# Optimization experiments

Hardware: AMD Instinct MI355X
Metric: run time of the kernel (lower is better)

Reference implementation:

```python
import jax, jax.numpy as jnp
import numpy as np

VOCAB = 50000
B, T, D_OUT = 32, 512, 256
E_DIMS = (300, 300, 200)


def setup_inputs() -> dict:
    key = jax.random.key(0)
    ks = jax.random.split(key, 8)
    ids = jax.random.randint(ks[0], (B, T), 0, VOCAB)
    E0 = jax.random.normal(ks[1], (VOCAB, E_DIMS[0]), dtype=jnp.float32)
    E1 = jax.random.normal(ks[2], (VOCAB, E_DIMS[1]), dtype=jnp.float32)
    E2 = jax.random.normal(ks[3], (VOCAB, E_DIMS[2]), dtype=jnp.float32)
    # Glorot-ish scaled projection weights
    W0 = jax.random.normal(ks[4], (E_DIMS[0], D_OUT), dtype=jnp.float32) / np.sqrt(E_DIMS[0])
    W1 = jax.random.normal(ks[5], (E_DIMS[1], D_OUT), dtype=jnp.float32) / np.sqrt(E_DIMS[1])
    W2 = jax.random.normal(ks[6], (E_DIMS[2], D_OUT), dtype=jnp.float32) / np.sqrt(E_DIMS[2])
    Wa = jax.random.normal(ks[7], (D_OUT, 1), dtype=jnp.float32) / np.sqrt(D_OUT)
    return {
        "ids": ids,
        "E0": E0, "E1": E1, "E2": E2,
        "W0": W0, "b0": jnp.zeros((D_OUT,), jnp.float32),
        "W1": W1, "b1": jnp.zeros((D_OUT,), jnp.float32),
        "W2": W2, "b2": jnp.zeros((D_OUT,), jnp.float32),
        "Wa": Wa, "ba": jnp.zeros((1,), jnp.float32),
    }


def reference(ids, E0, E1, E2, W0, b0, W1, b1, W2, b2, Wa, ba):
    # Per-source embedding gather + Dense projection -> [B, T, D_OUT]
    p0 = E0[ids] @ W0 + b0
    p1 = E1[ids] @ W1 + b1
    p2 = E2[ids] @ W2 + b2
    projected = jnp.stack([p0, p1, p2], axis=2)  # [B, T, n_emb, D]
    # Attention Dense(1) over D, softmax over the n_emb axis
    logits = jnp.einsum('btnd,do->btno', projected, Wa) + ba  # [B, T, n, 1]
    alphas = jax.nn.softmax(logits, axis=2)
    # Weighted combine: matmul(projected^T, alphas) then squeeze -> [B, T, D]
    out = jnp.einsum('btnd,btn->btd', projected, alphas[..., 0])
    return out
```

## Files before the change

### kernel.cpp

```cpp
#include <hip/hip_runtime.h>
#include <hip/hip_bf16.h>

typedef __attribute__((ext_vector_type(8))) short short8;
typedef __attribute__((ext_vector_type(4))) float floatx4;
typedef unsigned short ushort_t;
typedef unsigned int uint_t;

#define DOUT   256
#define KPAD   864
#define XPITCH 872
#define TB     32
#define NTOK   16384

static __device__ inline ushort_t f2bf(float f) {
    union { float f; uint_t u; } a; a.f = f;
    uint_t u = a.u;
    return (ushort_t)((u + 0x7FFFu + ((u >> 16) & 1u)) >> 16);
}
static __device__ inline uint_t pack2bf(float x, float y) {
    return (uint_t)f2bf(x) | ((uint_t)f2bf(y) << 16);
}

__global__ __launch_bounds__(64) void k_prep_u(
    const float* __restrict__ W0, const float* __restrict__ W1,
    const float* __restrict__ W2,
    const float* __restrict__ b0, const float* __restrict__ b1,
    const float* __restrict__ b2,
    const float* __restrict__ Wa, const float* __restrict__ ba,
    float* __restrict__ u, float* __restrict__ lb)
{
    int kp = blockIdx.x;
    int lane = threadIdx.x;
    const float* row = nullptr;
    if (kp < 320)       { if (kp < 300) row = W0 + kp * DOUT; }
    else if (kp < 640)  { int o = kp - 320; if (o < 300) row = W1 + o * DOUT; }
    else if (kp < 864)  { int o = kp - 640; if (o < 200) row = W2 + o * DOUT; }
    else                { int n = kp - 864; row = (n == 0) ? b0 : ((n == 1) ? b1 : b2); }
    float acc = 0.f;
    if (row) {
        for (int j = lane; j < DOUT; j += 64)
            acc += row[j] * Wa[j];
    }
    for (int off = 32; off > 0; off >>= 1) acc += __shfl_down(acc, off);
    if (lane == 0) {
        if (kp < 864) u[kp] = acc;
        else          lb[kp - 864] = acc + ba[0];
    }
}

__global__ __launch_bounds__(256) void k_prep_t(
    const float* __restrict__ W0, const float* __restrict__ W1,
    const float* __restrict__ W2, ushort_t* __restrict__ Wt)
{
    __shared__ ushort_t tile[32][256];
    int tid = threadIdx.x;
    int k0 = blockIdx.x * 32;
    for (int idx = tid; idx < 32 * 256; idx += 256) {
        int kk = idx >> 8, d = idx & 255;
        int kp = k0 + kk;
        float v = 0.f;
        const float* src = nullptr;
        if (kp < 320)      { if (kp < 300) src = W0 + kp * DOUT; }
        else if (kp < 640) { int o = kp - 320; if (o < 300) src = W1 + o * DOUT; }
        else               { int o = kp - 640; if (o < 200) src = W2 + o * DOUT; }
        if (src) v = src[d];
        tile[kk][d] = f2bf(v);
    }
    __syncthreads();
    int d = tid;
    #pragma unroll
    for (int g = 0; g < 4; ++g) {
        union { uint4 v; ushort_t s[8]; } p;
        #pragma unroll
        for (int j = 0; j < 8; ++j) p.s[j] = tile[g * 8 + j][d];
        *(uint4*)(Wt + (size_t)d * KPAD + k0 + g * 8) = p.v;
    }
}

#define MFMA_STEP(ACC, KC) {                                                   \
    short8 a0 = *(const short8*)&Xs[mrow][(KC) + kg8];                         \
    short8 a1 = *(const short8*)&Xs[16 + mrow][(KC) + kg8];                    \
    short8 bv0 = *(const short8*)(bp0 + (KC));                                 \
    short8 bv1 = *(const short8*)(bp1 + (KC));                                 \
    short8 bv2 = *(const short8*)(bp2 + (KC));                                 \
    short8 bv3 = *(const short8*)(bp3 + (KC));                                 \
    ACC[0][0] = __builtin_amdgcn_mfma_f32_16x16x32_bf16(a0, bv0, ACC[0][0], 0, 0, 0); \
    ACC[1][0] = __builtin_amdgcn_mfma_f32_16x16x32_bf16(a1, bv0, ACC[1][0], 0, 0, 0); \
    ACC[0][1] = __builtin_amdgcn_mfma_f32_16x16x32_bf16(a0, bv1, ACC[0][1], 0, 0, 0); \
    ACC[1][1] = __builtin_amdgcn_mfma_f32_16x16x32_bf16(a1, bv1, ACC[1][1], 0, 0, 0); \
    ACC[0][2] = __builtin_amdgcn_mfma_f32_16x16x32_bf16(a0, bv2, ACC[0][2], 0, 0, 0); \
    ACC[1][2] = __builtin_amdgcn_mfma_f32_16x16x32_bf16(a1, bv2, ACC[1][2], 0, 0, 0); \
    ACC[0][3] = __builtin_amdgcn_mfma_f32_16x16x32_bf16(a0, bv3, ACC[0][3], 0, 0, 0); \
    ACC[1][3] = __builtin_amdgcn_mfma_f32_16x16x32_bf16(a1, bv3, ACC[1][3], 0, 0, 0); \
}

__global__ __launch_bounds__(256, 2) void k_main(
    const int* __restrict__ ids,
    const float* __restrict__ E0, const float* __restrict__ E1,
    const float* __restrict__ E2,
    const float* __restrict__ b0, const float* __restrict__ b1,
    const float* __restrict__ b2,
    const float* __restrict__ u, const float* __restrict__ lb,
    const ushort_t* __restrict__ Wt,
    float* __restrict__ out)
{
    __shared__ __align__(16) ushort_t Xs[TB][XPITCH];
    __shared__ float uS[KPAD];
    __shared__ float alphaS[TB][4];

    int tid = threadIdx.x;
    int tok0 = blockIdx.x * TB;

    for (int i = tid; i < KPAD; i += 256) uS[i] = u[i];

    int trow = tid >> 3, sub = tid & 7;
    int id = ids[tok0 + trow];
    uint_t* Xd = (uint_t*)&Xs[trow][0];
    const float2* E0v = (const float2*)E0;
    const float2* E1v = (const float2*)E1;
    const float2* E2v = (const float2*)E2;
    for (int i = sub; i < 150; i += 8) { float2 t = E0v[(size_t)id * 150 + i]; Xd[i]       = pack2bf(t.x, t.y); }
    for (int i = sub; i < 150; i += 8) { float2 t = E1v[(size_t)id * 150 + i]; Xd[160 + i] = pack2bf(t.x, t.y); }
    for (int i = sub; i < 100; i += 8) { float2 t = E2v[(size_t)id * 100 + i]; Xd[320 + i] = pack2bf(t.x, t.y); }
    for (int i = 150 + sub; i < 160; i += 8) Xd[i] = 0u;
    for (int i = 310 + sub; i < 320; i += 8) Xd[i] = 0u;
    for (int i = 420 + sub; i < 436; i += 8) Xd[i] = 0u;
    __syncthreads();

    const ushort_t* xr = Xs[trow];
    float l0 = 0.f, l1 = 0.f, l2 = 0.f;
    for (int k = sub * 2; k < 320; k += 16) {
        uint_t p = *(const uint_t*)&xr[k];
        float2 uu = *(const float2*)&uS[k];
        l0 += __uint_as_float(p << 16) * uu.x + __uint_as_float(p & 0xFFFF0000u) * uu.y;
    }
    for (int k = 320 + sub * 2; k < 640; k += 16) {
        uint_t p = *(const uint_t*)&xr[k];
        float2 uu = *(const float2*)&uS[k];
        l1 += __uint_as_float(p << 16) * uu.x + __uint_as_float(p & 0xFFFF0000u) * uu.y;
    }
    for (int k = 640 + sub * 2; k < 864; k += 16) {
        uint_t p = *(const uint_t*)&xr[k];
        float2 uu = *(const float2*)&uS[k];
        l2 += __uint_as_float(p << 16) * uu.x + __uint_as_float(p & 0xFFFF0000u) * uu.y;
    }
    for (int off = 4; off > 0; off >>= 1) {
        l0 += __shfl_down(l0, off);
        l1 += __shfl_down(l1, off);
        l2 += __shfl_down(l2, off);
    }
    if (sub == 0) {
        l0 += lb[0]; l1 += lb[1]; l2 += lb[2];
        float m = fmaxf(l0, fmaxf(l1, l2));
        float e0 = __expf(l0 - m), e1 = __expf(l1 - m), e2 = __expf(l2 - m);
        float inv = 1.f / (e0 + e1 + e2);
        alphaS[trow][0] = e0 * inv;
        alphaS[trow][1] = e1 * inv;
        alphaS[trow][2] = e2 * inv;
    }
    __syncthreads();

    int lane = tid & 63;
    int w = tid >> 6;
    int mrow = lane & 15;
    int kg8 = (lane >> 4) * 8;

    const ushort_t* bp0 = Wt + (size_t)(w * 64 +  0 + mrow) * KPAD + kg8;
    const ushort_t* bp1 = Wt + (size_t)(w * 64 + 16 + mrow) * KPAD + kg8;
    const ushort_t* bp2 = Wt + (size_t)(w * 64 + 32 + mrow) * KPAD + kg8;
    const ushort_t* bp3 = Wt + (size_t)(w * 64 + 48 + mrow) * KPAD + kg8;

    floatx4 acc0[2][4], acc1[2][4], acc2[2][4];
    #pragma unroll
    for (int mt = 0; mt < 2; ++mt)
        #pragma unroll
        for (int nt = 0; nt < 4; ++nt) {
            floatx4 z = {0.f, 0.f, 0.f, 0.f};
            acc0[mt][nt] = z; acc1[mt][nt] = z; acc2[mt][nt] = z;
        }

    #pragma unroll
    for (int kc = 0; kc < 320; kc += 32)   MFMA_STEP(acc0, kc);
    #pragma unroll
    for (int kc = 320; kc < 640; kc += 32) MFMA_STEP(acc1, kc);
    #pragma unroll
    for (int kc = 640; kc < 864; kc += 32) MFMA_STEP(acc2, kc);

    float bb0[4], bb1[4], bb2[4];
    #pragma unroll
    for (int nt = 0; nt < 4; ++nt) {
        int n = w * 64 + nt * 16 + mrow;
        bb0[nt] = b0[n];
        bb1[nt] = b1[n];
        bb2[nt] = b2[n];
    }
    #pragma unroll
    for (int mt = 0; mt < 2; ++mt) {
        #pragma unroll
        for (int r = 0; r < 4; ++r) {
            int tok = mt * 16 + (lane >> 4) * 4 + r;
            float a0 = alphaS[tok][0], a1 = alphaS[tok][1], a2 = alphaS[tok][2];
            size_t rowoff = (size_t)(tok0 + tok) * DOUT;
            #pragma unroll
            for (int nt = 0; nt < 4; ++nt) {
                int n = w * 64 + nt * 16 + mrow;
                float v = a0 * (acc0[mt][nt][r] + bb0[nt])
                        + a1 * (acc1[mt][nt][r] + bb1[nt])
                        + a2 * (acc2[mt][nt][r] + bb2[nt]);
                out[rowoff + n] = v;
            }
        }
    }
}

extern "C" void kernel_launch(void* const* d_in, const int* in_sizes, int n_in,
                              void* d_out, int out_size, void* d_ws, size_t ws_size,
                              hipStream_t stream) {
    const int*   ids = (const int*)d_in[0];
    const float* E0  = (const float*)d_in[1];
    const float* E1  = (const float*)d_in[2];
    const float* E2  = (const float*)d_in[3];
    const float* W0  = (const float*)d_in[4];
    const float* b0  = (const float*)d_in[5];
    const float* W1  = (const float*)d_in[6];
    const float* b1  = (const float*)d_in[7];
    const float* W2  = (const float*)d_in[8];
    const float* b2  = (const float*)d_in[9];
    const float* Wa  = (const float*)d_in[10];
    const float* ba  = (const float*)d_in[11];

    float* u     = (float*)d_ws;
    float* lb    = u + KPAD;
    ushort_t* Wt = (ushort_t*)((char*)d_ws + 4096);

    k_prep_u<<<KPAD + 3, 64, 0, stream>>>(W0, W1, W2, b0, b1, b2, Wa, ba, u, lb);
    k_prep_t<<<KPAD / 32, 256, 0, stream>>>(W0, W1, W2, Wt);
    k_main<<<NTOK / TB, 256, 0, stream>>>(ids, E0, E1, E2, b0, b1, b2, u, lb, Wt,
                                          (float*)d_out);
}
```

Baseline: 214.2 us.

## Fuse logit computation into gather, widen loads, split MFMA over 8 waves

The two weight-prep kernels are merged into a single launch, with block index choosing between the transpose path and the Wa dot-product path. The main kernel now runs 512 threads per block with 16 threads per token. It gathers embedding rows with float4 loads and computes attention logits from the fp32 values during the gather. This removes the shared-memory u copy and the separate bf16 re-read pass. Each of the 8 waves computes 32 output columns instead of 64, which lowers accumulator registers and raises occupancy, at the cost of reading the A tile from LDS more often.

```diff
diff --git a/kernel.cpp b/kernel.cpp
--- a/kernel.cpp
+++ b/kernel.cpp
@@ -11,6 +11,8 @@
 #define XPITCH 872
 #define TB     32
 #define NTOK   16384
+#define NPREP_T 27
+#define NPREP_U 217
 
 static __device__ inline ushort_t f2bf(float f) {
     union { float f; uint_t u; } a; a.f = f;
@@ -21,59 +23,59 @@
     return (uint_t)f2bf(x) | ((uint_t)f2bf(y) << 16);
 }
 
-__global__ __launch_bounds__(64) void k_prep_u(
+__global__ __launch_bounds__(256) void k_prep(
     const float* __restrict__ W0, const float* __restrict__ W1,
     const float* __restrict__ W2,
     const float* __restrict__ b0, const float* __restrict__ b1,
     const float* __restrict__ b2,
     const float* __restrict__ Wa, const float* __restrict__ ba,
-    float* __restrict__ u, float* __restrict__ lb)
-{
-    int kp = blockIdx.x;
-    int lane = threadIdx.x;
-    const float* row = nullptr;
-    if (kp < 320)       { if (kp < 300) row = W0 + kp * DOUT; }
-    else if (kp < 640)  { int o = kp - 320; if (o < 300) row = W1 + o * DOUT; }
-    else if (kp < 864)  { int o = kp - 640; if (o < 200) row = W2 + o * DOUT; }
-    else                { int n = kp - 864; row = (n == 0) ? b0 : ((n == 1) ? b1 : b2); }
-    float acc = 0.f;
-    if (row) {
-        for (int j = lane; j < DOUT; j += 64)
-            acc += row[j] * Wa[j];
-    }
-    for (int off = 32; off > 0; off >>= 1) acc += __shfl_down(acc, off);
-    if (lane == 0) {
-        if (kp < 864) u[kp] = acc;
-        else          lb[kp - 864] = acc + ba[0];
-    }
-}
-
-__global__ __launch_bounds__(256) void k_prep_t(
-    const float* __restrict__ W0, const float* __restrict__ W1,
-    const float* __restrict__ W2, ushort_t* __restrict__ Wt)
+    float* __restrict__ u, float* __restrict__ lb, ushort_t* __restrict__ Wt)
 {
     __shared__ ushort_t tile[32][256];
     int tid = threadIdx.x;
-    int k0 = blockIdx.x * 32;
-    for (int idx = tid; idx < 32 * 256; idx += 256) {
-        int kk = idx >> 8, d = idx & 255;
-        int kp = k0 + kk;
-        float v = 0.f;
-        const float* src = nullptr;
-        if (kp < 320)      { if (kp < 300) src = W0 + kp * DOUT; }
-        else if (kp < 640) { int o = kp - 320; if (o < 300) src = W1 + o * DOUT; }
-        else               { int o = kp - 640; if (o < 200) src = W2 + o * DOUT; }
-        if (src) v = src[d];
-        tile[kk][d] = f2bf(v);
-    }
-    __syncthreads();
-    int d = tid;
-    #pragma unroll
-    for (int g = 0; g < 4; ++g) {
-        union { uint4 v; ushort_t s[8]; } p;
+    if (blockIdx.x < NPREP_T) {
+        int k0 = blockIdx.x * 32;
+        for (int idx = tid; idx < 32 * 256; idx += 256) {
+            int kk = idx >> 8, d = idx & 255;
+            int kp = k0 + kk;
+            float v = 0.f;
+            const float* src = nullptr;
+            if (kp < 320)      { if (kp < 300) src = W0 + kp * DOUT; }
+            else if (kp < 640) { int o = kp - 320; if (o < 300) src = W1 + o * DOUT; }
+            else               { int o = kp - 640; if (o < 200) src = W2 + o * DOUT; }
+            if (src) v = src[d];
+            tile[kk][d] = f2bf(v);
+        }
+        __syncthreads();
+        int d = tid;
         #pragma unroll
-        for (int j = 0; j < 8; ++j) p.s[j] = tile[g * 8 + j][d];
-        *(uint4*)(Wt + (size_t)d * KPAD + k0 + g * 8) = p.v;
+        for (int g = 0; g < 4; ++g) {
+            union { uint4 v; ushort_t s[8]; } p;
+            #pragma unroll
+            for (int j = 0; j < 8; ++j) p.s[j] = tile[g * 8 + j][d];
+            *(uint4*)(Wt + (size_t)d * KPAD + k0 + g * 8) = p.v;
+        }
+    } else {
+        int lane = tid & 63;
+        int w = tid >> 6;
+        int kp = (blockIdx.x - NPREP_T) * 4 + w;
+        if (kp > 866) return;
+        const float* row = nullptr;
+        if (kp < 320)       { if (kp < 300) row = W0 + kp * DOUT; }
+        else if (kp < 640)  { int o = kp - 320; if (o < 300) row = W1 + o * DOUT; }
+        else if (kp < 864)  { int o = kp - 640; if (o < 200) row = W2 + o * DOUT; }
+        else                { int n = kp - 864; row = (n == 0) ? b0 : ((n == 1) ? b1 : b2); }
+        float acc = 0.f;
+        if (row) {
+            #pragma unroll
+            for (int j = lane; j < DOUT; j += 64)
+                acc += row[j] * Wa[j];
+        }
+        for (int off = 32; off > 0; off >>= 1) acc += __shfl_down(acc, off);
+        if (lane == 0) {
+            if (kp < 864) u[kp] = acc;
+            else          lb[kp - 864] = acc + ba[0];
+        }
     }
 }
 
@@ -82,19 +84,13 @@
     short8 a1 = *(const short8*)&Xs[16 + mrow][(KC) + kg8];                    \
     short8 bv0 = *(const short8*)(bp0 + (KC));                                 \
     short8 bv1 = *(const short8*)(bp1 + (KC));                                 \
-    short8 bv2 = *(const short8*)(bp2 + (KC));                                 \
-    short8 bv3 = *(const short8*)(bp3 + (KC));                                 \
     ACC[0][0] = __builtin_amdgcn_mfma_f32_16x16x32_bf16(a0, bv0, ACC[0][0], 0, 0, 0); \
     ACC[1][0] = __builtin_amdgcn_mfma_f32_16x16x32_bf16(a1, bv0, ACC[1][0], 0, 0, 0); \
     ACC[0][1] = __builtin_amdgcn_mfma_f32_16x16x32_bf16(a0, bv1, ACC[0][1], 0, 0, 0); \
     ACC[1][1] = __builtin_amdgcn_mfma_f32_16x16x32_bf16(a1, bv1, ACC[1][1], 0, 0, 0); \
-    ACC[0][2] = __builtin_amdgcn_mfma_f32_16x16x32_bf16(a0, bv2, ACC[0][2], 0, 0, 0); \
-    ACC[1][2] = __builtin_amdgcn_mfma_f32_16x16x32_bf16(a1, bv2, ACC[1][2], 0, 0, 0); \
-    ACC[0][3] = __builtin_amdgcn_mfma_f32_16x16x32_bf16(a0, bv3, ACC[0][3], 0, 0, 0); \
-    ACC[1][3] = __builtin_amdgcn_mfma_f32_16x16x32_bf16(a1, bv3, ACC[1][3], 0, 0, 0); \
-}
-
-__global__ __launch_bounds__(256, 2) void k_main(
+}
+
+__global__ __launch_bounds__(512, 4) void k_main(
     const int* __restrict__ ids,
     const float* __restrict__ E0, const float* __restrict__ E1,
     const float* __restrict__ E2,
@@ -105,46 +101,47 @@
     float* __restrict__ out)
 {
     __shared__ __align__(16) ushort_t Xs[TB][XPITCH];
-    __shared__ float uS[KPAD];
     __shared__ float alphaS[TB][4];
 
     int tid = threadIdx.x;
     int tok0 = blockIdx.x * TB;
 
-    for (int i = tid; i < KPAD; i += 256) uS[i] = u[i];
-
-    int trow = tid >> 3, sub = tid & 7;
+    int trow = tid >> 4, sub = tid & 15;
     int id = ids[tok0 + trow];
-    uint_t* Xd = (uint_t*)&Xs[trow][0];
-    const float2* E0v = (const float2*)E0;
-    const float2* E1v = (const float2*)E1;
-    const float2* E2v = (const float2*)E2;
-    for (int i = sub; i < 150; i += 8) { float2 t = E0v[(size_t)id * 150 + i]; Xd[i]       = pack2bf(t.x, t.y); }
-    for (int i = sub; i < 150; i += 8) { float2 t = E1v[(size_t)id * 150 + i]; Xd[160 + i] = pack2bf(t.x, t.y); }
-    for (int i = sub; i < 100; i += 8) { float2 t = E2v[(size_t)id * 100 + i]; Xd[320 + i] = pack2bf(t.x, t.y); }
-    for (int i = 150 + sub; i < 160; i += 8) Xd[i] = 0u;
-    for (int i = 310 + sub; i < 320; i += 8) Xd[i] = 0u;
-    for (int i = 420 + sub; i < 436; i += 8) Xd[i] = 0u;
-    __syncthreads();
-
-    const ushort_t* xr = Xs[trow];
+    uint2* Xd2 = (uint2*)&Xs[trow][0];
+    const float4* E0v = (const float4*)E0;
+    const float4* E1v = (const float4*)E1;
+    const float4* E2v = (const float4*)E2;
     float l0 = 0.f, l1 = 0.f, l2 = 0.f;
-    for (int k = sub * 2; k < 320; k += 16) {
-        uint_t p = *(const uint_t*)&xr[k];
-        float2 uu = *(const float2*)&uS[k];
-        l0 += __uint_as_float(p << 16) * uu.x + __uint_as_float(p & 0xFFFF0000u) * uu.y;
-    }
-    for (int k = 320 + sub * 2; k < 640; k += 16) {
-        uint_t p = *(const uint_t*)&xr[k];
-        float2 uu = *(const float2*)&uS[k];
-        l1 += __uint_as_float(p << 16) * uu.x + __uint_as_float(p & 0xFFFF0000u) * uu.y;
-    }
-    for (int k = 640 + sub * 2; k < 864; k += 16) {
-        uint_t p = *(const uint_t*)&xr[k];
-        float2 uu = *(const float2*)&uS[k];
-        l2 += __uint_as_float(p << 16) * uu.x + __uint_as_float(p & 0xFFFF0000u) * uu.y;
-    }
-    for (int off = 4; off > 0; off >>= 1) {
+
+    #pragma unroll
+    for (int i = sub; i < 75; i += 16) {
+        float4 t = E0v[(size_t)id * 75 + i];
+        float4 uu = *(const float4*)(u + 4 * i);
+        l0 += t.x * uu.x + t.y * uu.y + t.z * uu.z + t.w * uu.w;
+        Xd2[i] = make_uint2(pack2bf(t.x, t.y), pack2bf(t.z, t.w));
+    }
+    #pragma unroll
+    for (int i = sub; i < 75; i += 16) {
+        float4 t = E1v[(size_t)id * 75 + i];
+        float4 uu = *(const float4*)(u + 320 + 4 * i);
+        l1 += t.x * uu.x + t.y * uu.y + t.z * uu.z + t.w * uu.w;
+        Xd2[80 + i] = make_uint2(pack2bf(t.x, t.y), pack2bf(t.z, t.w));
+    }
+    #pragma unroll
+    for (int i = sub; i < 50; i += 16) {
+        float4 t = E2v[(size_t)id * 50 + i];
+        float4 uu = *(const float4*)(u + 640 + 4 * i);
+        l2 += t.x * uu.x + t.y * uu.y + t.z * uu.z + t.w * uu.w;
+        Xd2[160 + i] = make_uint2(pack2bf(t.x, t.y), pack2bf(t.z, t.w));
+    }
+    uint2 z2 = make_uint2(0u, 0u);
+    for (int i = 75 + sub;  i < 80;  i += 16) Xd2[i] = z2;
+    for (int i = 155 + sub; i < 160; i += 16) Xd2[i] = z2;
+    for (int i = 210 + sub; i < 218; i += 16) Xd2[i] = z2;
+
+    #pragma unroll
+    for (int off = 8; off > 0; off >>= 1) {
         l0 += __shfl_down(l0, off);
         l1 += __shfl_down(l1, off);
         l2 += __shfl_down(l2, off);
@@ -165,16 +162,14 @@
     int mrow = lane & 15;
     int kg8 = (lane >> 4) * 8;
 
-    const ushort_t* bp0 = Wt + (size_t)(w * 64 +  0 + mrow) * KPAD + kg8;
-    const ushort_t* bp1 = Wt + (size_t)(w * 64 + 16 + mrow) * KPAD + kg8;
-    const ushort_t* bp2 = Wt + (size_t)(w * 64 + 32 + mrow) * KPAD + kg8;
-    const ushort_t* bp3 = Wt + (size_t)(w * 64 + 48 + mrow) * KPAD + kg8;
-
-    floatx4 acc0[2][4], acc1[2][4], acc2[2][4];
+    const ushort_t* bp0 = Wt + (size_t)(w * 32 +  0 + mrow) * KPAD + kg8;
+    const ushort_t* bp1 = Wt + (size_t)(w * 32 + 16 + mrow) * KPAD + kg8;
+
+    floatx4 acc0[2][2], acc1[2][2], acc2[2][2];
     #pragma unroll
     for (int mt = 0; mt < 2; ++mt)
         #pragma unroll
-        for (int nt = 0; nt < 4; ++nt) {
+        for (int nt = 0; nt < 2; ++nt) {
             floatx4 z = {0.f, 0.f, 0.f, 0.f};
             acc0[mt][nt] = z; acc1[mt][nt] = z; acc2[mt][nt] = z;
         }
@@ -186,10 +181,10 @@
     #pragma unroll
     for (int kc = 640; kc < 864; kc += 32) MFMA_STEP(acc2, kc);
 
-    float bb0[4], bb1[4], bb2[4];
-    #pragma unroll
-    for (int nt = 0; nt < 4; ++nt) {
-        int n = w * 64 + nt * 16 + mrow;
+    float bb0[2], bb1[2], bb2[2];
+    #pragma unroll
+    for (int nt = 0; nt < 2; ++nt) {
+        int n = w * 32 + nt * 16 + mrow;
         bb0[nt] = b0[n];
         bb1[nt] = b1[n];
         bb2[nt] = b2[n];
@@ -202,8 +197,8 @@
             float a0 = alphaS[tok][0], a1 = alphaS[tok][1], a2 = alphaS[tok][2];
             size_t rowoff = (size_t)(tok0 + tok) * DOUT;
             #pragma unroll
-            for (int nt = 0; nt < 4; ++nt) {
-                int n = w * 64 + nt * 16 + mrow;
+            for (int nt = 0; nt < 2; ++nt) {
+                int n = w * 32 + nt * 16 + mrow;
                 float v = a0 * (acc0[mt][nt][r] + bb0[nt])
                         + a1 * (acc1[mt][nt][r] + bb1[nt])
                         + a2 * (acc2[mt][nt][r] + bb2[nt]);
@@ -233,8 +228,8 @@
     float* lb    = u + KPAD;
     ushort_t* Wt = (ushort_t*)((char*)d_ws + 4096);
 
-    k_prep_u<<<KPAD + 3, 64, 0, stream>>>(W0, W1, W2, b0, b1, b2, Wa, ba, u, lb);
-    k_prep_t<<<KPAD / 32, 256, 0, stream>>>(W0, W1, W2, Wt);
-    k_main<<<NTOK / TB, 256, 0, stream>>>(ids, E0, E1, E2, b0, b1, b2, u, lb, Wt,
+    k_prep<<<NPREP_T + NPREP_U, 256, 0, stream>>>(W0, W1, W2, b0, b1, b2, Wa, ba,
+                                                  u, lb, Wt);
+    k_main<<<NTOK / TB, 512, 0, stream>>>(ids, E0, E1, E2, b0, b1, b2, u, lb, Wt,
                                           (float*)d_out);
 }
```

Measured after the change: 205.2 us. 4.2% less time.
